# Kernel optimization log

Hardware: AMD Instinct MI355X
Metric: run time of the kernel (lower is better)

## Reference

```python
import jax, jax.numpy as jnp
import numpy as np

NUM_HEADS = 16


def setup_inputs() -> dict:
    key = jax.random.key(0)
    ks = jax.random.split(key, 6)
    B, T, C = 2, 1024, 2048
    H, D = NUM_HEADS, C // NUM_HEADS
    Tc = 1024  # cached tokens
    return {
        "x": jax.random.normal(ks[0], (B, T, C), dtype=jnp.float32),
        "cache_k": jax.random.normal(ks[1], (B, H, Tc, D), dtype=jnp.float32),
        "cache_v": jax.random.normal(ks[2], (B, H, Tc, D), dtype=jnp.float32),
        "W_qkv": jax.random.normal(ks[3], (C, 3 * C), dtype=jnp.float32) * (C ** -0.5),
        "W_proj": jax.random.normal(ks[4], (C, C), dtype=jnp.float32) * (C ** -0.5),
        "b_proj": jnp.zeros((C,), dtype=jnp.float32),
        "seq_start": Tc,
    }


def reference(x, cache_k, cache_v, W_qkv, W_proj, b_proj, seq_start):
    B, T, C = x.shape
    H = NUM_HEADS
    D = C // H
    scale = D ** -0.5

    qkv = (x @ W_qkv).reshape(B, T, 3, H, D)
    # (B, H, T, D)
    q = jnp.transpose(qkv[:, :, 0], (0, 2, 1, 3))
    k = jnp.transpose(qkv[:, :, 1], (0, 2, 1, 3))
    v = jnp.transpose(qkv[:, :, 2], (0, 2, 1, 3))

    # append to KV cache along time axis
    k = jnp.concatenate([cache_k, k], axis=2)
    v = jnp.concatenate([cache_v, v], axis=2)
    k_len = k.shape[2]

    # causal mask on absolute positions: query_pos >= key_pos
    query_pos = seq_start + jnp.arange(T)
    key_pos = jnp.arange(k_len)
    causal = query_pos[:, None] >= key_pos[None, :]  # (T, k_len)

    attn = jnp.einsum("bhqd,bhkd->bhqk", q * scale, k)
    attn = jnp.where(causal[None, None], attn, -jnp.inf)
    attn = jax.nn.softmax(attn, axis=-1)

    out = jnp.einsum("bhqk,bhkd->bhqd", attn, v)
    out = jnp.transpose(out, (0, 2, 1, 3)).reshape(B, T, C)
    out = out @ W_proj + b_proj
    return out, k, v
```

## Files before the change

kernel.cpp:

```cpp
#include <hip/hip_runtime.h>
#include <hip/hip_bf16.h>

typedef __attribute__((ext_vector_type(8))) short bf16x8;
typedef __attribute__((ext_vector_type(4))) float f32x4;
typedef __attribute__((ext_vector_type(16))) float f32x16;

#define DI __device__ __forceinline__

static constexpr int Bb  = 2;
static constexpr int Tt  = 1024;
static constexpr int Cc  = 2048;
static constexpr int Hh  = 16;
static constexpr int Dd  = 128;
static constexpr int TC  = 1024;
static constexpr int CTX = 2048;
static constexpr int LDP = 2112;
static constexpr int VS  = 2080;
static constexpr float QSCALE = 0.08838834764831845f;

DI unsigned short f2bf(float f){
  unsigned u = __builtin_bit_cast(unsigned, f);
  u += 0x7FFFu + ((u >> 16) & 1u);
  return (unsigned short)(u >> 16);
}
DI float bf2f(unsigned short s){
  return __builtin_bit_cast(float, (unsigned)s << 16);
}
DI unsigned pk2(float a, float b){
  return (unsigned)f2bf(a) | ((unsigned)f2bf(b) << 16);
}
DI bf16x8 mk4(unsigned a, unsigned b, unsigned c, unsigned d){
  union{ unsigned u[4]; bf16x8 v; } x;
  x.u[0]=a; x.u[1]=b; x.u[2]=c; x.u[3]=d; return x.v;
}
DI f32x16 mfma32(bf16x8 a, bf16x8 b, f32x16 c){
  return __builtin_amdgcn_mfma_f32_32x32x16_bf16(a, b, c, 0, 0, 0);
}
#define MFMA16(a,b,c) __builtin_amdgcn_mfma_f32_16x16x32_bf16(a,b,c,0,0,0)
DI void gld16(const void* g, void* l){
  __builtin_amdgcn_global_load_lds(
      (const __attribute__((address_space(1))) unsigned int*)g,
      (__attribute__((address_space(3))) unsigned int*)l, 16, 0, 0);
}
DI unsigned ldsoff(const void* p){
  return (unsigned)(size_t)(const __attribute__((address_space(3))) void*)p;
}
template<int OFF>
DI bf16x8 dsr(unsigned addr){
  bf16x8 v;
  if constexpr (OFF == 0)
    asm volatile("ds_read_b128 %0, %1" : "=v"(v) : "v"(addr));
  else
    asm volatile("ds_read_b128 %0, %1 offset:%2" : "=v"(v) : "v"(addr), "i"(OFF));
  return v;
}
#define BARNC   asm volatile("s_barrier")
#define LGKM0   asm volatile("s_waitcnt lgkmcnt(0)")
#define VMCNT4  asm volatile("s_waitcnt vmcnt(4)")
#define VMCNT0  asm volatile("s_waitcnt vmcnt(0)")
#define SBAR    __builtin_amdgcn_sched_barrier(0)

DI void transpose_body(const float* in, unsigned short* out,
                       int R, int C, int ostride, int r0, int c0, int mode,
                       unsigned short (*tile)[33]){
  int tx = threadIdx.x & 31, ty = threadIdx.x >> 5;
#pragma unroll
  for(int i=0;i<4;i++){
    int r = r0 + ty + i*8;
    tile[ty + i*8][tx] = f2bf(in[(size_t)r * C + c0 + tx]);
  }
  __syncthreads();
#pragma unroll
  for(int i=0;i<4;i++){
    int c = c0 + ty + i*8;
    int k = r0 + tx;
    int kp;
    if(mode == 0)
      kp = (k & ~24) | ((((k>>3)&3) ^ ((c>>1)&3)) << 3);
    else
      kp = (k & ~56) | ((((k>>3)&7) ^ (c&7)) << 3);
    out[(size_t)c * ostride + kp] = tile[tx][ty + i*8];
  }
}

__global__ __launch_bounds__(256) void fused_pre_k(
    const float* __restrict__ W_qkv, unsigned short* __restrict__ WqkvT,
    const float4* __restrict__ x4, unsigned short* __restrict__ xbf,
    const float4* __restrict__ ck, const float4* __restrict__ cv,
    float4* __restrict__ ok, float4* __restrict__ ov,
    unsigned short* __restrict__ Kws){
  __shared__ unsigned short tile[32][33];
  int bid = blockIdx.x;
  if(bid < 12288){
    int bx = bid % 192, by = bid / 192;
    transpose_body(W_qkv, WqkvT, 2048, 6144, LDP, by*32, bx*32, 1, tile);
  } else if(bid < 16384){
    int idx = (bid - 12288) * 256 + threadIdx.x;
    int m = idx >> 9;
    int c4 = (idx & 511) * 4;
    float4 v = x4[idx];
    int cp = ((((c4>>3) ^ (m&7)) << 3)) | (c4 & 7);
    uint2 p; p.x = pk2(v.x, v.y); p.y = pk2(v.z, v.w);
    *(uint2*)(xbf + (size_t)m * LDP + cp) = p;
  } else {
    int idx = (bid - 16384) * 256 + threadIdx.x;
    const int per = TC * Dd / 4;
    int bh = idx / per, r = idx - bh * per;
    int dst = bh * (CTX * Dd / 4) + r;
    float4 kv = ck[idx];
    ok[dst] = kv;
    ov[dst] = cv[idx];
    int key = r >> 5, dq = (r & 31) * 4;
    int dp = (((dq>>3) ^ (key&7)) << 3) | (dq & 7);
    uint2 p; p.x = pk2(kv.x, kv.y); p.y = pk2(kv.z, kv.w);
    *(uint2*)(Kws + ((size_t)bh * CTX + key) * Dd + dp) = p;
  }
}

__global__ __launch_bounds__(256) void fused_mid_k(
    const float* __restrict__ out_v, unsigned short* __restrict__ Vt_ws,
    const float* __restrict__ W_proj, unsigned short* __restrict__ WprojT){
  __shared__ unsigned short tile[32][33];
  int bid = blockIdx.x;
  if(bid < 8192){
    int z = bid >> 8, rem = bid & 255;
    int bx = rem & 3, by = rem >> 2;
    transpose_body(out_v + (size_t)z*2048*128, Vt_ws + (size_t)z*128*VS,
                   2048, 128, VS, by*32, bx*32, 1, tile);
  } else {
    int b2 = bid - 8192;
    int bx = b2 & 63, by = b2 >> 6;
    transpose_body(W_proj, WprojT, 2048, 2048, LDP, by*32, bx*32, 0, tile);
  }
}

__global__ __launch_bounds__(256, 2) void gemm8_k(
    const unsigned short* __restrict__ A, const unsigned short* __restrict__ BT,
    unsigned short* __restrict__ q_ws, float* __restrict__ out_k,
    float* __restrict__ out_v, unsigned short* __restrict__ Kws){
  __shared__ unsigned short lds[32768];
  int tid = threadIdx.x, lane = tid & 63, w = tid >> 6;
  int lr = lane & 15, lg = lane >> 4;
  int wm = w >> 1, wn = w & 1;
  int bid = blockIdx.x;
  int swz = (bid & 7) * 96 + (bid >> 3);
  int m0 = (swz & 15) * 128;
  int n0 = (swz >> 4) * 128;

  int r8 = lane >> 3, c8 = (lane & 7) * 8;
  const unsigned short* Asrc = A  + (size_t)(m0 + w*16 + r8)*LDP + c8;
  const unsigned short* Bsrc = BT + (size_t)(n0 + w*16 + r8)*LDP + c8;
  unsigned short* ldsA = lds;
  unsigned short* ldsB = lds + 16384;

  auto stgA = [&](int b, int h, int kt){
    const unsigned short* s = Asrc + (size_t)(h*64)*LDP + kt*64;
    unsigned short* d = ldsA + b*8192 + h*4096 + w*1024;
    gld16(s, d);
    gld16(s + (size_t)8*LDP, d + 512);
  };
  auto stgB = [&](int b, int h, int kt){
    const unsigned short* s = Bsrc + (size_t)(h*64)*LDP + kt*64;
    unsigned short* d = ldsB + b*8192 + h*4096 + w*1024;
    gld16(s, d);
    gld16(s + (size_t)8*LDP, d + 512);
  };

  unsigned LB   = ldsoff(lds);
  unsigned apAb = LB + (unsigned)(wm*64 + lr)*128;
  unsigned apBb = LB + 32768u + (unsigned)(wn*64 + lr)*128;
  unsigned ua0b = (unsigned)(( lg      ^ (lr & 7)) * 16);
  unsigned ua1b = (unsigned)(((4 + lg) ^ (lr & 7)) * 16);

  f32x4 acc[4][4];
#pragma unroll
  for(int i=0;i<4;i++)
#pragma unroll
    for(int j=0;j<4;j++) acc[i][j] = (f32x4){0.f,0.f,0.f,0.f};
  bf16x8 bfr[4][2];

  stgA(0,0,0); stgA(0,1,0); stgB(0,0,0); stgB(0,1,0); stgB(1,0,1); stgB(1,1,1);
  SBAR;
  VMCNT4;
  BARNC;

#define PHASE(BUF, Q, STAGE, VM)                                           \
  {                                                                        \
    unsigned a0 = apAb + (BUF)*16384u + (Q)*2048u + ua0b;                  \
    unsigned a1 = apAb + (BUF)*16384u + (Q)*2048u + ua1b;                  \
    bf16x8 a00 = dsr<0>(a0);                                               \
    bf16x8 a01 = dsr<0>(a1);                                               \
    if((Q) == 0){                                                          \
      unsigned b0 = apBb + (BUF)*16384u + ua0b;                            \
      unsigned b1 = apBb + (BUF)*16384u + ua1b;                            \
      bfr[0][0] = dsr<0>(b0);    bfr[1][0] = dsr<2048>(b0);                \
      bfr[2][0] = dsr<4096>(b0); bfr[3][0] = dsr<6144>(b0);                \
      bfr[0][1] = dsr<0>(b1);    bfr[1][1] = dsr<2048>(b1);                \
      bfr[2][1] = dsr<4096>(b1); bfr[3][1] = dsr<6144>(b1);                \
    }                                                                      \
    SBAR;                                                                  \
    STAGE;                                                                 \
    SBAR;                                                                  \
    BARNC;                                                                 \
    LGKM0;                                                                 \
    SBAR;                                                                  \
    __builtin_amdgcn_s_setprio(1);                                         \
    _Pragma("unroll")                                                      \
    for(int ni=0;ni<4;ni++)                                                \
      acc[(Q)][ni] = MFMA16(a00, bfr[ni][0], acc[(Q)][ni]);                \
    _Pragma("unroll")                                                      \
    for(int ni=0;ni<4;ni++)                                                \
      acc[(Q)][ni] = MFMA16(a01, bfr[ni][1], acc[(Q)][ni]);                \
    __builtin_amdgcn_s_setprio(0);                                         \
    SBAR;                                                                  \
    VM;                                                                    \
    BARNC;                                                                 \
  }

#pragma unroll 1
  for(int i=0;i<16;i++){
    int t1 = 2*i+1, t2 = (2*i+2)&31, t3 = (2*i+3)&31;
    PHASE(0, 0, stgA(1,0,t1), );
    PHASE(0, 1, stgA(1,1,t1), );
    PHASE(0, 2, stgB(0,0,t2), );
    PHASE(0, 3, stgB(0,1,t2), VMCNT4);
    PHASE(1, 0, stgA(0,0,t2), );
    PHASE(1, 1, stgA(0,1,t2), );
    PHASE(1, 2, stgB(1,0,t3), );
    PHASE(1, 3, stgB(1,1,t3), VMCNT4);
  }
#undef PHASE
  asm volatile("s_waitcnt vmcnt(0)" ::: "memory");

#pragma unroll
  for(int mi=0;mi<4;mi++){
#pragma unroll
    for(int ni=0;ni<4;ni++){
      int n = n0 + wn*64 + ni*16 + lr;
      int seg = n >> 11;
      int h = (n >> 7) & 15, d = n & 127;
#pragma unroll
      for(int r=0;r<4;r++){
        int mrow = m0 + wm*64 + mi*16 + lg*4 + r;
        float v = acc[mi][ni][r];
        int b = mrow >> 10, t = mrow & 1023;
        if(seg == 0){
          q_ws[((size_t)(b*Hh + h)*Tt + t)*Dd + d] = f2bf(v * QSCALE);
        } else if(seg == 1){
          int key = TC + t;
          size_t base = (size_t)(b*Hh + h)*CTX + key;
          out_k[base*Dd + d] = v;
          int dp = (((d>>3) ^ (key&7)) << 3) | (d & 7);
          Kws[base*Dd + dp] = f2bf(v);
        } else {
          out_v[((size_t)(b*Hh + h)*CTX + TC + t)*Dd + d] = v;
        }
      }
    }
  }
}

__global__ __launch_bounds__(256) void gemmp_k(
    const unsigned short* __restrict__ A, const unsigned short* __restrict__ BT,
    const float* __restrict__ bias, float* __restrict__ outp){
  constexpr int K = 2048;
  __shared__ unsigned short Al[2][128*32];
  __shared__ unsigned short Bl[2][128*32];
  int tid = threadIdx.x, lane = tid & 63, w = tid >> 6;
  int lr = lane & 15, lg = lane >> 4;
  int m0 = blockIdx.x * 128, n0 = blockIdx.y * 128;
  int wr = (w >> 1) * 64, wc = (w & 1) * 64;
  int swz = (lg ^ ((lr >> 1) & 3)) << 3;

  unsigned baseAb = ldsoff(Al) + (unsigned)(((wr + lr)*32 + swz)*2);
  unsigned baseBb = ldsoff(Bl) + (unsigned)(((wc + lr)*32 + swz)*2);

  f32x4 acc[4][4];
#pragma unroll
  for(int i=0;i<4;i++)
#pragma unroll
    for(int j=0;j<4;j++) acc[i][j] = (f32x4){0.f,0.f,0.f,0.f};

  auto stage = [&](int buf, int k0){
#pragma unroll
    for(int li=0; li<2; li++){
      int rb = w*32 + li*16;
      gld16(A  + (size_t)(m0 + rb + (lane>>2))*LDP + k0 + (lane&3)*8, &Al[buf][rb*32]);
      gld16(BT + (size_t)(n0 + rb + (lane>>2))*LDP + k0 + (lane&3)*8, &Bl[buf][rb*32]);
    }
  };
  stage(0, 0);
  int buf = 0;
#pragma unroll 1
  for(int k0 = 0; k0 < K; k0 += 32){
    SBAR;
    if(k0 + 32 < K){
      stage(buf^1, k0 + 32);
      SBAR;
      VMCNT4;
    } else {
      SBAR;
      VMCNT0;
    }
    BARNC;
    unsigned aA = baseAb + (unsigned)buf*8192u;
    unsigned aB = baseBb + (unsigned)buf*8192u;
    bf16x8 af[4], bfr[4];
    af[0]  = dsr<0>(aA);    af[1]  = dsr<1024>(aA);
    af[2]  = dsr<2048>(aA); af[3]  = dsr<3072>(aA);
    bfr[0] = dsr<0>(aB);    bfr[1] = dsr<1024>(aB);
    bfr[2] = dsr<2048>(aB); bfr[3] = dsr<3072>(aB);
    LGKM0;
    SBAR;
    __builtin_amdgcn_s_setprio(1);
#pragma unroll
    for(int mi=0;mi<4;mi++)
#pragma unroll
      for(int ni=0;ni<4;ni++)
        acc[mi][ni] = MFMA16(af[mi], bfr[ni], acc[mi][ni]);
    __builtin_amdgcn_s_setprio(0);
    SBAR;
    BARNC;
    buf ^= 1;
  }

#pragma unroll
  for(int mi=0;mi<4;mi++){
#pragma unroll
    for(int ni=0;ni<4;ni++){
      int n = n0 + wc + ni*16 + lr;
#pragma unroll
      for(int r=0;r<4;r++){
        int mrow = m0 + wr + mi*16 + lg*4 + r;
        outp[(size_t)mrow * Cc + n] = acc[mi][ni][r] + bias[n];
      }
    }
  }
}

__global__ __launch_bounds__(256, 2) void attn_k(
    const unsigned short* __restrict__ q_ws,
    const unsigned short* __restrict__ Kws,
    const unsigned short* __restrict__ Vt,
    float* __restrict__ O0, unsigned short* __restrict__ O1b,
    float* __restrict__ ml){
  __shared__ unsigned short Kl[2][64*128];
  __shared__ unsigned short Vl[2][128*64];
  int tid = threadIdx.x, lane = tid & 63, w = tid >> 6;
  int l31 = lane & 31, hi = lane >> 5, r7 = l31 & 7;
  int qt = blockIdx.x, split = blockIdx.y, bh = blockIdx.z;
  int q0b = qt * 128, qw0 = q0b + w * 32;
  const unsigned short* Kb = Kws + (size_t)bh * CTX * Dd;
  const unsigned short* Vb = Vt  + (size_t)bh * Dd * VS;

  const unsigned short* qp = q_ws + ((size_t)bh * Tt + qw0 + l31) * Dd + hi * 8;
  bf16x8 qf[8];
#pragma unroll
  for(int ks=0;ks<8;ks++) qf[ks] = *(const bf16x8*)(qp + ks*16);

  f32x16 o[4];
#pragma unroll
  for(int dt=0;dt<4;dt++)
#pragma unroll
    for(int r=0;r<16;r++) o[dt][r] = 0.f;
  float m = -3e38f, l = 0.f;

  int nts = ((TC + q0b + 128) >> 6) >> 1;

  auto stageK = [&](int buf, int j0){
#pragma unroll
    for(int li=0; li<4; li++){
      gld16(Kb + (size_t)(j0 + w*16 + li*4 + (lane>>4))*Dd + (lane&15)*8,
            &Kl[buf][(w*16 + li*4)*128]);
    }
  };
  auto stageV = [&](int buf, int j0){
#pragma unroll
    for(int li=0; li<4; li++){
      gld16(Vb + (size_t)(w*32 + li*8 + (lane>>3))*VS + j0 + (lane&7)*8,
            &Vl[buf][(w*32 + li*8)*64]);
    }
  };

  stageK(0, split*64); stageV(0, split*64);
  __syncthreads();
  int buf = 0;
#pragma unroll 1
  for(int t = 0; t < nts; t++){
    int j0 = (2*t + split) * 64;
    if(t + 1 < nts){ stageK(buf^1, j0 + 128); stageV(buf^1, j0 + 128); }

    if(j0 <= TC + qw0 + 31){
      f32x16 s0, s1;
#pragma unroll
      for(int r=0;r<16;r++){ s0[r] = 0.f; s1[r] = 0.f; }
#pragma unroll
      for(int ks=0; ks<8; ks++){
        int ub = ((ks*2 + hi) ^ r7) << 3;
        bf16x8 kf0 = *(const bf16x8*)&Kl[buf][l31*128 + ub];
        bf16x8 kf1 = *(const bf16x8*)&Kl[buf][(32+l31)*128 + ub];
        s0 = mfma32(kf0, qf[ks], s0);
        s1 = mfma32(kf1, qf[ks], s1);
      }
      int qabs = TC + qw0 + l31;
      if(j0 + 63 > TC + qw0){
#pragma unroll
        for(int r=0;r<16;r++){
          int kk = (r&3) + 8*(r>>2) + 4*hi;
          if(j0 + kk > qabs)      s0[r] = -1e30f;
          if(j0 + 32 + kk > qabs) s1[r] = -1e30f;
        }
      }
      float tm = fmaxf(s0[0], s1[0]);
#pragma unroll
      for(int r=1;r<16;r++) tm = fmaxf(tm, fmaxf(s0[r], s1[r]));
      tm = fmaxf(tm, __shfl_xor(tm, 32, 64));
      if(!__all(tm - m <= 8.f)){
        float mn = fmaxf(m, tm);
        float alpha = __expf(m - mn);
        m = mn;
        l *= alpha;
        float ar[16];
#pragma unroll
        for(int r=0;r<16;r++){
          int kk = (r&3) + 8*(r>>2) + 4*hi;
          ar[r] = __shfl(alpha, kk, 64);
        }
#pragma unroll
        for(int dt=0;dt<4;dt++)
#pragma unroll
          for(int r=0;r<16;r++) o[dt][r] *= ar[r];
      }
#pragma unroll
      for(int r=0;r<16;r++){ s0[r] = __expf(s0[r] - m); s1[r] = __expf(s1[r] - m); }
      float ts = 0.f;
#pragma unroll
      for(int r=0;r<16;r++) ts += s0[r] + s1[r];
      ts += __shfl_xor(ts, 32, 64);
      l += ts;
#pragma unroll
      for(int ks16=0; ks16<4; ks16++){
        f32x16 p = (ks16 & 2) ? s1 : s0;
        int fb = (ks16 & 1) * 8;
        unsigned e0 = pk2(p[fb+0], p[fb+1]);
        unsigned e1 = pk2(p[fb+2], p[fb+3]);
        unsigned e2 = pk2(p[fb+4], p[fb+5]);
        unsigned e3 = pk2(p[fb+6], p[fb+7]);
        unsigned x0 = __shfl_xor(e0, 32, 64);
        unsigned x1 = __shfl_xor(e1, 32, 64);
        unsigned x2 = __shfl_xor(e2, 32, 64);
        unsigned x3 = __shfl_xor(e3, 32, 64);
        bf16x8 pa = mk4(hi ? x2 : e0, hi ? x3 : e1, hi ? e2 : x0, hi ? e3 : x1);
        int ub = ((ks16*2 + hi) ^ r7) << 3;
#pragma unroll
        for(int dt=0; dt<4; dt++){
          bf16x8 vf = *(const bf16x8*)&Vl[buf][(dt*32 + l31)*64 + ub];
          o[dt] = mfma32(pa, vf, o[dt]);
        }
      }
    }
    __syncthreads();
    buf ^= 1;
  }

  if(split == 0){
#pragma unroll
    for(int dt=0; dt<4; dt++)
#pragma unroll
      for(int r=0; r<16; r++){
        int q = qw0 + (r&3) + 8*(r>>2) + 4*hi;
        O0[((size_t)bh*Tt + q)*Dd + dt*32 + l31] = o[dt][r];
      }
  } else {
#pragma unroll
    for(int dt=0; dt<4; dt++)
#pragma unroll
      for(int r=0; r<16; r++){
        int q = qw0 + (r&3) + 8*(r>>2) + 4*hi;
        O1b[((size_t)bh*Tt + q)*Dd + dt*32 + l31] = f2bf(o[dt][r]);
      }
  }
  if(lane < 32){
    float* mlp = ml + (((size_t)split*32 + bh)*Tt + qw0 + l31)*2;
    mlp[0] = m; mlp[1] = l;
  }
}

__global__ __launch_bounds__(256) void combine_k(
    const float* __restrict__ O0, const unsigned short* __restrict__ O1b,
    const float* __restrict__ ml, unsigned short* __restrict__ attn_ws){
  int tid = threadIdx.x;
  int d = tid & 127, rl = tid >> 7;
  int row = blockIdx.x * 2 + rl;
  int bh = row >> 10, t = row & 1023;
  const float* p0 = ml + ((size_t)bh * Tt + t) * 2;
  const float* p1 = ml + (((size_t)32 + bh) * Tt + t) * 2;
  float m0 = p0[0], l0 = p0[1], m1 = p1[0], l1 = p1[1];
  float M = fmaxf(m0, m1);
  float e0 = __expf(m0 - M), e1 = __expf(m1 - M);
  float inv = 1.f / (l0*e0 + l1*e1);
  size_t off = (size_t)row * Dd + d;
  float v = (O0[off]*e0 + bf2f(O1b[off])*e1) * inv;
  int b = bh >> 4, h = bh & 15;
  int mrow = b * Tt + t;
  int c = h * Dd + d;
  int cp = (c & ~24) | ((((c>>3)&3) ^ ((mrow>>1)&3)) << 3);
  attn_ws[(size_t)mrow * LDP + cp] = f2bf(v);
}

extern "C" void kernel_launch(void* const* d_in, const int* in_sizes, int n_in,
                              void* d_out, int out_size, void* d_ws, size_t ws_size,
                              hipStream_t stream){
  const float* x       = (const float*)d_in[0];
  const float* cache_k = (const float*)d_in[1];
  const float* cache_v = (const float*)d_in[2];
  const float* W_qkv   = (const float*)d_in[3];
  const float* W_proj  = (const float*)d_in[4];
  const float* b_proj  = (const float*)d_in[5];

  float* out   = (float*)d_out;
  float* out_k = out   + (size_t)Bb*Tt*Cc;
  float* out_v = out_k + (size_t)Bb*Hh*CTX*Dd;

  if(ws_size < (size_t)67108864) return;
  char* ws = (char*)d_ws;
  unsigned short* WqkvT  = (unsigned short*)(ws);
  unsigned short* Vt_ws  = (unsigned short*)(ws);
  unsigned short* attn_ws= (unsigned short*)(ws);
  unsigned short* WprojT = (unsigned short*)(ws + 17039360);
  unsigned short* Kws    = (unsigned short*)(ws + 25952256);
  unsigned short* q_ws   = (unsigned short*)(ws + 42729472);
  unsigned short* x_bf   = (unsigned short*)(ws + 51118080);
  unsigned short* O1b    = (unsigned short*)(ws + 51118080);
  float*          ml     = (float*)(ws + 59768832);
  float*          O0     = out;

  fused_pre_k<<<dim3(20480), 256, 0, stream>>>(
      W_qkv, WqkvT, (const float4*)x, x_bf,
      (const float4*)cache_k, (const float4*)cache_v,
      (float4*)out_k, (float4*)out_v, Kws);
  gemm8_k<<<dim3(768), 256, 0, stream>>>(x_bf, WqkvT, q_ws, out_k, out_v, Kws);
  fused_mid_k<<<dim3(12288), 256, 0, stream>>>(out_v, Vt_ws, W_proj, WprojT);
  attn_k<<<dim3(8,2,32), 256, 0, stream>>>(q_ws, Kws, Vt_ws, O0, O1b, ml);
  combine_k<<<dim3(16384), 256, 0, stream>>>(O0, O1b, ml, attn_ws);
  gemmp_k<<<dim3(16,16), 256, 0, stream>>>(attn_ws, WprojT, b_proj, out);
}
```

Before: 200.3 us.

## Replace QKV GEMM with templated double-buffered GEMM shared with projection

Removes the hand-scheduled gemm8_k (64-wide K stages, quarter-phase MFMA pipeline, 64KB LDS, 2 waves/SIMD bound) and uses a templated version of the projection GEMM (32-wide K double buffer, 32KB LDS, launch bound 4) for both the QKV and output projections. The templated kernel gains an L2-friendly block swizzle and an EPI switch for the QKV scatter epilogue. The weight-transpose and x-conversion swizzles switch to the mode matching the 32-wide LDS layout. This trades the deeper software pipeline for higher occupancy and less code.

```diff
diff --git a/kernel.cpp b/kernel.cpp
--- a/kernel.cpp
+++ b/kernel.cpp
@@ -93,13 +93,13 @@
   int bid = blockIdx.x;
   if(bid < 12288){
     int bx = bid % 192, by = bid / 192;
-    transpose_body(W_qkv, WqkvT, 2048, 6144, LDP, by*32, bx*32, 1, tile);
+    transpose_body(W_qkv, WqkvT, 2048, 6144, LDP, by*32, bx*32, 0, tile);
   } else if(bid < 16384){
     int idx = (bid - 12288) * 256 + threadIdx.x;
     int m = idx >> 9;
     int c4 = (idx & 511) * 4;
     float4 v = x4[idx];
-    int cp = ((((c4>>3) ^ (m&7)) << 3)) | (c4 & 7);
+    int cp = (c4 & ~24) | ((((c4>>3)&3) ^ ((m>>1)&3)) << 3);
     uint2 p; p.x = pk2(v.x, v.y); p.y = pk2(v.z, v.w);
     *(uint2*)(xbf + (size_t)m * LDP + cp) = p;
   } else {
@@ -134,146 +134,27 @@
   }
 }
 
-__global__ __launch_bounds__(256, 2) void gemm8_k(
+template<int EPI, int NT>
+__global__ __launch_bounds__(256, 4) void gemm_t(
     const unsigned short* __restrict__ A, const unsigned short* __restrict__ BT,
     unsigned short* __restrict__ q_ws, float* __restrict__ out_k,
-    float* __restrict__ out_v, unsigned short* __restrict__ Kws){
-  __shared__ unsigned short lds[32768];
-  int tid = threadIdx.x, lane = tid & 63, w = tid >> 6;
-  int lr = lane & 15, lg = lane >> 4;
-  int wm = w >> 1, wn = w & 1;
-  int bid = blockIdx.x;
-  int swz = (bid & 7) * 96 + (bid >> 3);
-  int m0 = (swz & 15) * 128;
-  int n0 = (swz >> 4) * 128;
-
-  int r8 = lane >> 3, c8 = (lane & 7) * 8;
-  const unsigned short* Asrc = A  + (size_t)(m0 + w*16 + r8)*LDP + c8;
-  const unsigned short* Bsrc = BT + (size_t)(n0 + w*16 + r8)*LDP + c8;
-  unsigned short* ldsA = lds;
-  unsigned short* ldsB = lds + 16384;
-
-  auto stgA = [&](int b, int h, int kt){
-    const unsigned short* s = Asrc + (size_t)(h*64)*LDP + kt*64;
-    unsigned short* d = ldsA + b*8192 + h*4096 + w*1024;
-    gld16(s, d);
-    gld16(s + (size_t)8*LDP, d + 512);
-  };
-  auto stgB = [&](int b, int h, int kt){
-    const unsigned short* s = Bsrc + (size_t)(h*64)*LDP + kt*64;
-    unsigned short* d = ldsB + b*8192 + h*4096 + w*1024;
-    gld16(s, d);
-    gld16(s + (size_t)8*LDP, d + 512);
-  };
-
-  unsigned LB   = ldsoff(lds);
-  unsigned apAb = LB + (unsigned)(wm*64 + lr)*128;
-  unsigned apBb = LB + 32768u + (unsigned)(wn*64 + lr)*128;
-  unsigned ua0b = (unsigned)(( lg      ^ (lr & 7)) * 16);
-  unsigned ua1b = (unsigned)(((4 + lg) ^ (lr & 7)) * 16);
-
-  f32x4 acc[4][4];
-#pragma unroll
-  for(int i=0;i<4;i++)
-#pragma unroll
-    for(int j=0;j<4;j++) acc[i][j] = (f32x4){0.f,0.f,0.f,0.f};
-  bf16x8 bfr[4][2];
-
-  stgA(0,0,0); stgA(0,1,0); stgB(0,0,0); stgB(0,1,0); stgB(1,0,1); stgB(1,1,1);
-  SBAR;
-  VMCNT4;
-  BARNC;
-
-#define PHASE(BUF, Q, STAGE, VM)                                           \
-  {                                                                        \
-    unsigned a0 = apAb + (BUF)*16384u + (Q)*2048u + ua0b;                  \
-    unsigned a1 = apAb + (BUF)*16384u + (Q)*2048u + ua1b;                  \
-    bf16x8 a00 = dsr<0>(a0);                                               \
-    bf16x8 a01 = dsr<0>(a1);                                               \
-    if((Q) == 0){                                                          \
-      unsigned b0 = apBb + (BUF)*16384u + ua0b;                            \
-      unsigned b1 = apBb + (BUF)*16384u + ua1b;                            \
-      bfr[0][0] = dsr<0>(b0);    bfr[1][0] = dsr<2048>(b0);                \
-      bfr[2][0] = dsr<4096>(b0); bfr[3][0] = dsr<6144>(b0);                \
-      bfr[0][1] = dsr<0>(b1);    bfr[1][1] = dsr<2048>(b1);                \
-      bfr[2][1] = dsr<4096>(b1); bfr[3][1] = dsr<6144>(b1);                \
-    }                                                                      \
-    SBAR;                                                                  \
-    STAGE;                                                                 \
-    SBAR;                                                                  \
-    BARNC;                                                                 \
-    LGKM0;                                                                 \
-    SBAR;                                                                  \
-    __builtin_amdgcn_s_setprio(1);                                         \
-    _Pragma("unroll")                                                      \
-    for(int ni=0;ni<4;ni++)                                                \
-      acc[(Q)][ni] = MFMA16(a00, bfr[ni][0], acc[(Q)][ni]);                \
-    _Pragma("unroll")                                                      \
-    for(int ni=0;ni<4;ni++)                                                \
-      acc[(Q)][ni] = MFMA16(a01, bfr[ni][1], acc[(Q)][ni]);                \
-    __builtin_amdgcn_s_setprio(0);                                         \
-    SBAR;                                                                  \
-    VM;                                                                    \
-    BARNC;                                                                 \
-  }
-
-#pragma unroll 1
-  for(int i=0;i<16;i++){
-    int t1 = 2*i+1, t2 = (2*i+2)&31, t3 = (2*i+3)&31;
-    PHASE(0, 0, stgA(1,0,t1), );
-    PHASE(0, 1, stgA(1,1,t1), );
-    PHASE(0, 2, stgB(0,0,t2), );
-    PHASE(0, 3, stgB(0,1,t2), VMCNT4);
-    PHASE(1, 0, stgA(0,0,t2), );
-    PHASE(1, 1, stgA(0,1,t2), );
-    PHASE(1, 2, stgB(1,0,t3), );
-    PHASE(1, 3, stgB(1,1,t3), VMCNT4);
-  }
-#undef PHASE
-  asm volatile("s_waitcnt vmcnt(0)" ::: "memory");
-
-#pragma unroll
-  for(int mi=0;mi<4;mi++){
-#pragma unroll
-    for(int ni=0;ni<4;ni++){
-      int n = n0 + wn*64 + ni*16 + lr;
-      int seg = n >> 11;
-      int h = (n >> 7) & 15, d = n & 127;
-#pragma unroll
-      for(int r=0;r<4;r++){
-        int mrow = m0 + wm*64 + mi*16 + lg*4 + r;
-        float v = acc[mi][ni][r];
-        int b = mrow >> 10, t = mrow & 1023;
-        if(seg == 0){
-          q_ws[((size_t)(b*Hh + h)*Tt + t)*Dd + d] = f2bf(v * QSCALE);
-        } else if(seg == 1){
-          int key = TC + t;
-          size_t base = (size_t)(b*Hh + h)*CTX + key;
-          out_k[base*Dd + d] = v;
-          int dp = (((d>>3) ^ (key&7)) << 3) | (d & 7);
-          Kws[base*Dd + dp] = f2bf(v);
-        } else {
-          out_v[((size_t)(b*Hh + h)*CTX + TC + t)*Dd + d] = v;
-        }
-      }
-    }
-  }
-}
-
-__global__ __launch_bounds__(256) void gemmp_k(
-    const unsigned short* __restrict__ A, const unsigned short* __restrict__ BT,
+    float* __restrict__ out_v, unsigned short* __restrict__ Kws,
     const float* __restrict__ bias, float* __restrict__ outp){
   constexpr int K = 2048;
   __shared__ unsigned short Al[2][128*32];
   __shared__ unsigned short Bl[2][128*32];
   int tid = threadIdx.x, lane = tid & 63, w = tid >> 6;
   int lr = lane & 15, lg = lane >> 4;
-  int m0 = blockIdx.x * 128, n0 = blockIdx.y * 128;
+  constexpr int NWG = 16 * NT;
+  int bid = blockIdx.x;
+  int swz = (bid & 7) * (NWG/8) + (bid >> 3);
+  int m0 = (swz & 15) * 128;
+  int n0 = (swz >> 4) * 128;
   int wr = (w >> 1) * 64, wc = (w & 1) * 64;
-  int swz = (lg ^ ((lr >> 1) & 3)) << 3;
-
-  unsigned baseAb = ldsoff(Al) + (unsigned)(((wr + lr)*32 + swz)*2);
-  unsigned baseBb = ldsoff(Bl) + (unsigned)(((wc + lr)*32 + swz)*2);
+  int fsw = (lg ^ ((lr >> 1) & 3)) << 3;
+
+  unsigned baseAb = ldsoff(Al) + (unsigned)(((wr + lr)*32 + fsw)*2);
+  unsigned baseBb = ldsoff(Bl) + (unsigned)(((wc + lr)*32 + fsw)*2);
 
   f32x4 acc[4][4];
 #pragma unroll
@@ -332,7 +213,25 @@
 #pragma unroll
       for(int r=0;r<4;r++){
         int mrow = m0 + wr + mi*16 + lg*4 + r;
-        outp[(size_t)mrow * Cc + n] = acc[mi][ni][r] + bias[n];
+        float v = acc[mi][ni][r];
+        if constexpr (EPI == 0){
+          int seg = n >> 11;
+          int h = (n >> 7) & 15, d = n & 127;
+          int b = mrow >> 10, t = mrow & 1023;
+          if(seg == 0){
+            q_ws[((size_t)(b*Hh + h)*Tt + t)*Dd + d] = f2bf(v * QSCALE);
+          } else if(seg == 1){
+            int key = TC + t;
+            size_t base = (size_t)(b*Hh + h)*CTX + key;
+            out_k[base*Dd + d] = v;
+            int dp = (((d>>3) ^ (key&7)) << 3) | (d & 7);
+            Kws[base*Dd + dp] = f2bf(v);
+          } else {
+            out_v[((size_t)(b*Hh + h)*CTX + TC + t)*Dd + d] = v;
+          }
+        } else {
+          outp[(size_t)mrow * Cc + n] = v + bias[n];
+        }
       }
     }
   }
@@ -539,9 +438,11 @@
       W_qkv, WqkvT, (const float4*)x, x_bf,
       (const float4*)cache_k, (const float4*)cache_v,
       (float4*)out_k, (float4*)out_v, Kws);
-  gemm8_k<<<dim3(768), 256, 0, stream>>>(x_bf, WqkvT, q_ws, out_k, out_v, Kws);
+  gemm_t<0,48><<<dim3(768), 256, 0, stream>>>(x_bf, WqkvT, q_ws, out_k, out_v, Kws,
+                                              nullptr, nullptr);
   fused_mid_k<<<dim3(12288), 256, 0, stream>>>(out_v, Vt_ws, W_proj, WprojT);
   attn_k<<<dim3(8,2,32), 256, 0, stream>>>(q_ws, Kws, Vt_ws, O0, O1b, ml);
   combine_k<<<dim3(16384), 256, 0, stream>>>(O0, O1b, ml, attn_ws);
-  gemmp_k<<<dim3(16,16), 256, 0, stream>>>(attn_ws, WprojT, b_proj, out);
-}
+  gemm_t<1,16><<<dim3(256), 256, 0, stream>>>(attn_ws, WprojT, nullptr, nullptr, nullptr,
+                                              nullptr, b_proj, out);
+}
```

Result: slower. 209.5 us (+4.6%).
